# Performance work log

Measured on AMD Instinct MI355X. Metric: run time of the kernel, lower is better.

## Reference

```python
import jax, jax.numpy as jnp
import numpy as np

B, S, E = 8, 4096, 512
QKV, H = 512, 8
D = QKV // H  # head_dim = 64
EPS = 1e-6


def setup_inputs() -> dict:
    key = jax.random.key(0)
    ks = jax.random.split(key, 9)
    sc_in = 1.0 / np.sqrt(E)
    sc_qkv = 1.0 / np.sqrt(QKV)
    # Linear weights stored as [in, out] so y = x @ W + b (equivalent to torch x @ W_t.T + b)
    return {
        "x": jax.random.normal(ks[0], (B, S, E), dtype=jnp.float32),
        "Wq": jax.random.uniform(ks[1], (E, QKV), jnp.float32, -sc_in, sc_in),
        "bq": jax.random.uniform(ks[2], (QKV,), jnp.float32, -sc_in, sc_in),
        "Wk": jax.random.uniform(ks[3], (E, QKV), jnp.float32, -sc_in, sc_in),
        "bk": jax.random.uniform(ks[4], (QKV,), jnp.float32, -sc_in, sc_in),
        "Wv": jax.random.uniform(ks[5], (E, QKV), jnp.float32, -sc_in, sc_in),
        "bv": jax.random.uniform(ks[6], (QKV,), jnp.float32, -sc_in, sc_in),
        "Wo": jax.random.uniform(ks[7], (QKV, E), jnp.float32, -sc_qkv, sc_qkv),
        "bo": jax.random.uniform(ks[8], (E,), jnp.float32, -sc_qkv, sc_qkv),
    }


def feature_map(t):
    # elu(x) + 1 (always positive features)
    return jax.nn.elu(t) + 1.0


def reference(x, Wq, bq, Wk, bk, Wv, bv, Wo, bo):
    bs, seqlen, _ = x.shape
    q = (x @ Wq + bq).reshape(bs, seqlen, H, D)
    k = (x @ Wk + bk).reshape(bs, seqlen, H, D)
    v = (x @ Wv + bv).reshape(bs, seqlen, H, D)
    q = feature_map(q)
    k = feature_map(k)
    # kv: [n, h, m, d] -- per-head outer-product accumulation over sequence
    kv = jnp.einsum('nshd,nshm->nhmd', k, v)
    # normalizer z: [n, l, h]
    z = 1.0 / (jnp.einsum('nlhd,nhd->nlh', q, k.sum(axis=1)) + EPS)
    out = jnp.einsum('nlhd,nhmd,nlh->nlhm', q, kv, z)
    out = out.reshape(bs, seqlen, QKV)
    return out @ Wo + bo
```

## Files before the change

kernel.cpp:

```cpp
#include <hip/hip_runtime.h>
#include <hip/hip_bf16.h>


typedef __bf16 bf16x8 __attribute__((ext_vector_type(8)));
typedef float  f32x4  __attribute__((ext_vector_type(4)));

__device__ __forceinline__ float b2f(unsigned short u) {
    unsigned int x = ((unsigned int)u) << 16;
    return __builtin_bit_cast(float, x);
}
__device__ __forceinline__ unsigned short f2b(float f) {
    unsigned int u = __builtin_bit_cast(unsigned int, f);
    unsigned int r = (u + 0x7FFFu + ((u >> 16) & 1u)) >> 16;
    return (unsigned short)r;
}
__device__ __forceinline__ void load_lds16(const unsigned short* g, unsigned short* l) {
    __builtin_amdgcn_global_load_lds(
        (const __attribute__((address_space(1))) void*)g,
        (__attribute__((address_space(3))) void*)l, 16, 0, 0);
}

__global__ void prep_kernel(const float* __restrict__ x,
                            const float* __restrict__ w0, const float* __restrict__ w1,
                            const float* __restrict__ w2, const float* __restrict__ w3,
                            unsigned short* __restrict__ xb, unsigned short* __restrict__ wt,
                            float* __restrict__ ksg) {
    __shared__ float tile[64][65];
    int t = threadIdx.x;
    if (blockIdx.x >= 256) {
        int i = (blockIdx.x - 256) * 256 + t;
        float4 v = ((const float4*)x)[i];
        ushort4 o;
        o.x = f2b(v.x); o.y = f2b(v.y); o.z = f2b(v.z); o.w = f2b(v.w);
        ((ushort4*)xb)[i] = o;
        return;
    }
    int idx = blockIdx.x;
    if (idx < 16) ksg[idx * 256 + t] = 0.f;
    int bz = idx >> 6, by = (idx >> 3) & 7, bx = idx & 7;
    const float* src = (bz == 0) ? w0 : (bz == 1) ? w1 : (bz == 2) ? w2 : w3;
    unsigned short* dst = wt + (size_t)bz * 512 * 512;
    int rb = by * 64, cb = bx * 64;
    #pragma unroll
    for (int i = 0; i < 16; i++) {
        int c = t + i * 256; int r = c >> 6, cc = c & 63;
        tile[r][cc] = src[(rb + r) * 512 + cb + cc];
    }
    __syncthreads();
    #pragma unroll
    for (int i = 0; i < 16; i++) {
        int c = t + i * 256; int r = c >> 6, cc = c & 63;
        dst[(cb + r) * 512 + rb + cc] = f2b(tile[cc][r]);
    }
}

__global__ __launch_bounds__(256, 4) void gemm_qkv_kernel(
        const unsigned short* __restrict__ xb, const unsigned short* __restrict__ wt,
        const float* __restrict__ bq, const float* __restrict__ bk, const float* __restrict__ bv,
        unsigned short* __restrict__ qb, unsigned short* __restrict__ kT,
        unsigned short* __restrict__ vT, float* __restrict__ ksg) {
    int g = blockIdx.x;
    int xcd = g & 7, slot = g >> 3;
    int mtile = xcd * 32 + slot / 12;
    int tn = slot % 12;
    int tensor = tn >> 2, ntile = tn & 3;
    const unsigned short* Bt = wt + (size_t)tensor * 512 * 512;
    const float* bias = tensor == 0 ? bq : tensor == 1 ? bk : bv;
    bool act = tensor < 2;

    __shared__ __align__(16) unsigned short sA[128 * 64];
    __shared__ __align__(16) unsigned short sB[128 * 64];
    const int tid  = threadIdx.x;
    const int wave = tid >> 6, lane = tid & 63;
    const int wm = wave >> 1, wn = wave & 1;
    const int quad = lane >> 4, l16 = lane & 15;
    const int mbase = mtile * 128, nbase = ntile * 128;
    const int rsub = lane >> 3;
    const int coff = (((lane & 7) ^ rsub) << 3);

    f32x4 acc[4][4];
    #pragma unroll
    for (int i = 0; i < 4; i++)
        #pragma unroll
        for (int j = 0; j < 4; j++) acc[i][j] = (f32x4){0.f, 0.f, 0.f, 0.f};

    for (int kb = 0; kb < 512; kb += 64) {
        #pragma unroll
        for (int t = 0; t < 4; t++) {
            int r0 = t * 32 + wave * 8;
            load_lds16(&xb[(size_t)(mbase + r0 + rsub) * 512 + kb + coff], &sA[r0 * 64]);
            load_lds16(&Bt[(size_t)(nbase + r0 + rsub) * 512 + kb + coff], &sB[r0 * 64]);
        }
        __syncthreads();
        #pragma unroll
        for (int ko = 0; ko < 64; ko += 32) {
            bf16x8 af[4], bfr[4];
            int pg = ((quad + (ko >> 3)) ^ (l16 & 7)) << 3;
            #pragma unroll
            for (int f = 0; f < 4; f++)
                af[f] = *(const bf16x8*)&sA[(wm * 64 + f * 16 + l16) * 64 + pg];
            #pragma unroll
            for (int f = 0; f < 4; f++)
                bfr[f] = *(const bf16x8*)&sB[(wn * 64 + f * 16 + l16) * 64 + pg];
            #pragma unroll
            for (int i = 0; i < 4; i++)
                #pragma unroll
                for (int j = 0; j < 4; j++)
                    acc[i][j] = __builtin_amdgcn_mfma_f32_16x16x32_bf16(af[i], bfr[j], acc[i][j], 0, 0, 0);
        }
        __syncthreads();
    }
    if (tensor == 0) {
        #pragma unroll
        for (int i = 0; i < 4; i++)
            #pragma unroll
            for (int j = 0; j < 4; j++) {
                int gcol = nbase + wn * 64 + j * 16 + l16;
                float bv = bias[gcol];
                #pragma unroll
                for (int r = 0; r < 4; r++) {
                    int grow = mbase + wm * 64 + i * 16 + quad * 4 + r;
                    float v = acc[i][j][r] + bv;
                    v = v > 0.f ? v + 1.f : __expf(v);
                    qb[(size_t)grow * 512 + gcol] = f2b(v);
                }
            }
    } else {
        unsigned short* T = (tensor == 1) ? kT : vT;
        float csum[4] = {0.f, 0.f, 0.f, 0.f};
        #pragma unroll
        for (int i = 0; i < 4; i++)
            #pragma unroll
            for (int j = 0; j < 4; j++) {
                int gcol = nbase + wn * 64 + j * 16 + l16;
                int h = gcol >> 6, d = gcol & 63;
                float bv = bias[gcol];
                int grow0 = mbase + wm * 64 + i * 16 + quad * 4;
                int b = grow0 >> 12, s0 = grow0 & 4095;
                ushort4 o;
                #pragma unroll
                for (int r = 0; r < 4; r++) {
                    float v = acc[i][j][r] + bv;
                    if (act) { v = v > 0.f ? v + 1.f : __expf(v); csum[j] += v; }
                    ((unsigned short*)&o)[r] = f2b(v);
                }
                *(ushort4*)&T[(((size_t)b * 8 + h) * 64 + d) * 4096 + s0] = o;
            }
        if (act) {
            int b = mbase >> 12;
            #pragma unroll
            for (int j = 0; j < 4; j++) {
                float s = csum[j];
                s += __shfl_xor(s, 16, 64);
                s += __shfl_xor(s, 32, 64);
                if (quad == 0) {
                    int gcol = nbase + wn * 64 + j * 16 + l16;
                    atomicAdd(&ksg[b * 512 + gcol], s);
                }
            }
        }
    }
}

__global__ __launch_bounds__(256, 4) void kv_kernel(
        const unsigned short* __restrict__ kT, const unsigned short* __restrict__ vT,
        float* __restrict__ kvp) {
    int bh = blockIdx.x >> 3, sc = blockIdx.x & 7;
    const int tid = threadIdx.x;
    const int wave = tid >> 6, lane = tid & 63;
    const int wm = wave >> 1, wn = wave & 1;
    const int quad = lane >> 4, l16 = lane & 15;
    const int rsub = lane >> 3;
    const int coff = (((lane & 7) ^ rsub) << 3);
    __shared__ __align__(16) unsigned short sV[64 * 64];
    __shared__ __align__(16) unsigned short sK[64 * 64];

    f32x4 acc[2][2];
    #pragma unroll
    for (int i = 0; i < 2; i++)
        #pragma unroll
        for (int j = 0; j < 2; j++) acc[i][j] = (f32x4){0.f, 0.f, 0.f, 0.f};
    size_t base = (size_t)bh * 64 * 4096 + sc * 512;

    for (int kb = 0; kb < 8; kb++) {
        int s0 = kb * 64;
        #pragma unroll
        for (int t = 0; t < 2; t++) {
            int r0 = t * 32 + wave * 8;
            load_lds16(&vT[base + (size_t)(r0 + rsub) * 4096 + s0 + coff], &sV[r0 * 64]);
            load_lds16(&kT[base + (size_t)(r0 + rsub) * 4096 + s0 + coff], &sK[r0 * 64]);
        }
        __syncthreads();
        #pragma unroll
        for (int ko = 0; ko < 64; ko += 32) {
            bf16x8 af[2], bfr[2];
            int pg = ((quad + (ko >> 3)) ^ (l16 & 7)) << 3;
            #pragma unroll
            for (int f = 0; f < 2; f++)
                af[f] = *(const bf16x8*)&sV[(wm * 32 + f * 16 + l16) * 64 + pg];
            #pragma unroll
            for (int f = 0; f < 2; f++)
                bfr[f] = *(const bf16x8*)&sK[(wn * 32 + f * 16 + l16) * 64 + pg];
            #pragma unroll
            for (int i = 0; i < 2; i++)
                #pragma unroll
                for (int j = 0; j < 2; j++)
                    acc[i][j] = __builtin_amdgcn_mfma_f32_16x16x32_bf16(af[i], bfr[j], acc[i][j], 0, 0, 0);
        }
        __syncthreads();
    }
    float* kvout = kvp + ((size_t)sc * 64 + bh) * 4096;
    #pragma unroll
    for (int i = 0; i < 2; i++)
        #pragma unroll
        for (int j = 0; j < 2; j++)
            #pragma unroll
            for (int r = 0; r < 4; r++) {
                int m = wm * 32 + i * 16 + quad * 4 + r;
                int d = wn * 32 + j * 16 + l16;
                kvout[m * 64 + d] = acc[i][j][r];
            }
}

__global__ __launch_bounds__(256) void mid_kernel(
        const float* __restrict__ kvp, unsigned short* __restrict__ kvb) {
    int bh = blockIdx.x >> 2, part = blockIdx.x & 3;
    int tid = threadIdx.x;
    int idx = (part * 256 + tid) * 4;
    float s0 = 0.f, s1 = 0.f, s2 = 0.f, s3 = 0.f;
    #pragma unroll
    for (int sc = 0; sc < 8; sc++) {
        float4 v = *(const float4*)&kvp[((size_t)sc * 64 + bh) * 4096 + idx];
        s0 += v.x; s1 += v.y; s2 += v.z; s3 += v.w;
    }
    ushort4 o; o.x = f2b(s0); o.y = f2b(s1); o.z = f2b(s2); o.w = f2b(s3);
    *(ushort4*)&kvb[(size_t)bh * 4096 + idx] = o;
}

__global__ __launch_bounds__(256, 2) void fused_out_kernel(
        const unsigned short* __restrict__ qb,
        const unsigned short* __restrict__ kvb, const float* __restrict__ ksg,
        const unsigned short* __restrict__ wto, const float* __restrict__ bo,
        float* __restrict__ out) {
    int g = blockIdx.x;
    int xcd = g & 7, slot = g >> 3;
    int mtile = xcd * 32 + (slot >> 1);
    int np = slot & 1;

    __shared__ __align__(16) unsigned short sQ[128 * 64];
    __shared__ __align__(16) unsigned short sWo[2][128 * 64];
    __shared__ __align__(16) unsigned short sKV[64 * 64];
    __shared__ __align__(16) unsigned short sO1[128 * 64];
    __shared__ float sKsum[512];
    __shared__ float sZ[128];
    const int tid  = threadIdx.x;
    const int wave = tid >> 6, lane = tid & 63;
    const int wm = wave >> 1, wn = wave & 1;
    const int quad = lane >> 4, l16 = lane & 15;
    const int mbase = mtile * 128, nbase = np * 256;
    const int b = mtile >> 5;
    const int rsub = lane >> 3;
    const int coff = (((lane & 7) ^ rsub) << 3);

    sKsum[tid]       = ksg[b * 512 + tid];
    sKsum[tid + 256] = ksg[b * 512 + 256 + tid];

    f32x4 accm[2][4][4];
    #pragma unroll
    for (int n = 0; n < 2; n++)
        #pragma unroll
        for (int i = 0; i < 4; i++)
            #pragma unroll
            for (int j = 0; j < 4; j++) accm[n][i][j] = (f32x4){0.f, 0.f, 0.f, 0.f};

    for (int h = 0; h < 8; h++) {
        #pragma unroll
        for (int t = 0; t < 4; t++) {
            int r0 = t * 32 + wave * 8;
            load_lds16(&qb[(size_t)(mbase + r0 + rsub) * 512 + h * 64 + coff], &sQ[r0 * 64]);
            load_lds16(&wto[(size_t)(nbase + r0 + rsub) * 512 + h * 64 + coff], &sWo[0][r0 * 64]);
            load_lds16(&wto[(size_t)(nbase + 128 + r0 + rsub) * 512 + h * 64 + coff], &sWo[1][r0 * 64]);
        }
        #pragma unroll
        for (int t = 0; t < 2; t++) {
            int r0 = t * 32 + wave * 8;
            load_lds16(&kvb[(size_t)(b * 8 + h) * 4096 + (r0 + rsub) * 64 + coff], &sKV[r0 * 64]);
        }
        __syncthreads();
        {
            int row = tid >> 1, half = tid & 1;
            const float* ksh = &sKsum[h * 64];
            float dsum = 0.f;
            #pragma unroll
            for (int g2 = 0; g2 < 4; g2++) {
                int G = half * 4 + g2;
                uint4 w = *(const uint4*)&sQ[row * 64 + ((G ^ (row & 7)) << 3)];
                const unsigned int* qp = (const unsigned int*)&w;
                #pragma unroll
                for (int u = 0; u < 4; u++) {
                    int c = G * 8 + u * 2;
                    dsum += __builtin_bit_cast(float, qp[u] << 16)        * ksh[c];
                    dsum += __builtin_bit_cast(float, qp[u] & 0xFFFF0000u) * ksh[c + 1];
                }
            }
            dsum += __shfl_xor(dsum, 1, 64);
            if (!half) sZ[row] = 1.f / (dsum + 1e-6f);
        }
        __syncthreads();
        f32x4 acco[4][2];
        #pragma unroll
        for (int f = 0; f < 4; f++)
            #pragma unroll
            for (int j = 0; j < 2; j++) acco[f][j] = (f32x4){0.f, 0.f, 0.f, 0.f};
        #pragma unroll
        for (int ko = 0; ko < 64; ko += 32) {
            bf16x8 af[4], bfr[2];
            int pg = ((quad + (ko >> 3)) ^ (l16 & 7)) << 3;
            #pragma unroll
            for (int f = 0; f < 4; f++)
                af[f] = *(const bf16x8*)&sQ[(wm * 64 + f * 16 + l16) * 64 + pg];
            #pragma unroll
            for (int j = 0; j < 2; j++)
                bfr[j] = *(const bf16x8*)&sKV[(wn * 32 + j * 16 + l16) * 64 + pg];
            #pragma unroll
            for (int f = 0; f < 4; f++)
                #pragma unroll
                for (int j = 0; j < 2; j++)
                    acco[f][j] = __builtin_amdgcn_mfma_f32_16x16x32_bf16(af[f], bfr[j], acco[f][j], 0, 0, 0);
        }
        #pragma unroll
        for (int f = 0; f < 4; f++)
            #pragma unroll
            for (int j = 0; j < 2; j++)
                #pragma unroll
                for (int r = 0; r < 4; r++) {
                    int row = wm * 64 + f * 16 + quad * 4 + r;
                    int col = wn * 32 + j * 16 + l16;
                    float v = acco[f][j][r] * sZ[row];
                    int grp = col >> 3;
                    sO1[row * 64 + ((grp ^ (row & 7)) << 3) + (col & 7)] = f2b(v);
                }
        __syncthreads();
        #pragma unroll
        for (int ko = 0; ko < 64; ko += 32) {
            bf16x8 af[4], bfr0[4], bfr1[4];
            int pg = ((quad + (ko >> 3)) ^ (l16 & 7)) << 3;
            #pragma unroll
            for (int f = 0; f < 4; f++)
                af[f] = *(const bf16x8*)&sO1[(wm * 64 + f * 16 + l16) * 64 + pg];
            #pragma unroll
            for (int f = 0; f < 4; f++) {
                bfr0[f] = *(const bf16x8*)&sWo[0][(wn * 64 + f * 16 + l16) * 64 + pg];
                bfr1[f] = *(const bf16x8*)&sWo[1][(wn * 64 + f * 16 + l16) * 64 + pg];
            }
            #pragma unroll
            for (int i = 0; i < 4; i++)
                #pragma unroll
                for (int j = 0; j < 4; j++) {
                    accm[0][i][j] = __builtin_amdgcn_mfma_f32_16x16x32_bf16(af[i], bfr0[j], accm[0][i][j], 0, 0, 0);
                    accm[1][i][j] = __builtin_amdgcn_mfma_f32_16x16x32_bf16(af[i], bfr1[j], accm[1][i][j], 0, 0, 0);
                }
        }
        __syncthreads();
    }
    #pragma unroll
    for (int n = 0; n < 2; n++)
        #pragma unroll
        for (int i = 0; i < 4; i++)
            #pragma unroll
            for (int j = 0; j < 4; j++) {
                int gcol = nbase + n * 128 + wn * 64 + j * 16 + l16;
                float bv = bo[gcol];
                #pragma unroll
                for (int r = 0; r < 4; r++) {
                    int grow = mbase + wm * 64 + i * 16 + quad * 4 + r;
                    out[(size_t)grow * 512 + gcol] = accm[n][i][j][r] + bv;
                }
            }
}

extern "C" void kernel_launch(void* const* d_in, const int* in_sizes, int n_in,
                              void* d_out, int out_size, void* d_ws, size_t ws_size,
                              hipStream_t stream) {
    const float* x  = (const float*)d_in[0];
    const float* Wq = (const float*)d_in[1];
    const float* bq = (const float*)d_in[2];
    const float* Wk = (const float*)d_in[3];
    const float* bk = (const float*)d_in[4];
    const float* Wv = (const float*)d_in[5];
    const float* bv = (const float*)d_in[6];
    const float* Wo = (const float*)d_in[7];
    const float* bo = (const float*)d_in[8];
    float* out = (float*)d_out;

    char* wsb = (char*)d_ws;
    char* ob  = (char*)d_out;
    unsigned short* vT  = (unsigned short*)ob;
    unsigned short* xb  = (unsigned short*)(ob + 33554432ull);
    float*          kvp = (float*)(ob + 33554432ull);
    unsigned short* qb  = (unsigned short*)wsb;
    unsigned short* kT  = (unsigned short*)(wsb + 33554432ull);
    unsigned short* wt  = (unsigned short*)(wsb + 67108864ull);
    unsigned short* kvb = (unsigned short*)(wsb + 69206016ull);
    float*          ksg = (float*)(wsb + 69730304ull);

    prep_kernel<<<16640, 256, 0, stream>>>(x, Wq, Wk, Wv, Wo, xb, wt, ksg);
    gemm_qkv_kernel<<<3072, 256, 0, stream>>>(xb, wt, bq, bk, bv, qb, kT, vT, ksg);
    kv_kernel<<<512, 256, 0, stream>>>(kT, vT, kvp);
    mid_kernel<<<256, 256, 0, stream>>>(kvp, kvb);
    fused_out_kernel<<<512, 256, 0, stream>>>(qb, kvb, ksg,
            wt + 3ull * 512 * 512, bo, out);
}
```

Measured before the change: 242.5 us.

## Atomically reduce KV partials, drop mid kernel, double-buffer kv_kernel loads

The kv_kernel now accumulates its per-chunk partial KV products straight into a zeroed fp32 global buffer with atomicAdd. This removes the separate mid_kernel reduction launch and the intermediate partial buffer. The fused output kernel converts the fp32 KV to bf16 while staging it into LDS. kv_kernel also double-buffers its LDS tiles with explicit waitcnt and barriers so the next chunk's loads overlap compute. The costs are atomic contention (8 chunks per bh), a register-path load instead of a direct LDS load, and non-deterministic summation order.

```diff
diff --git a/kernel.cpp b/kernel.cpp
--- a/kernel.cpp
+++ b/kernel.cpp
@@ -24,7 +24,7 @@
                             const float* __restrict__ w0, const float* __restrict__ w1,
                             const float* __restrict__ w2, const float* __restrict__ w3,
                             unsigned short* __restrict__ xb, unsigned short* __restrict__ wt,
-                            float* __restrict__ ksg) {
+                            float* __restrict__ ksg, float* __restrict__ kvg) {
     __shared__ float tile[64][65];
     int t = threadIdx.x;
     if (blockIdx.x >= 256) {
@@ -37,6 +37,7 @@
     }
     int idx = blockIdx.x;
     if (idx < 16) ksg[idx * 256 + t] = 0.f;
+    ((float4*)kvg)[idx * 256 + t] = (float4){0.f, 0.f, 0.f, 0.f};
     int bz = idx >> 6, by = (idx >> 3) & 7, bx = idx & 7;
     const float* src = (bz == 0) ? w0 : (bz == 1) ? w1 : (bz == 2) ? w2 : w3;
     unsigned short* dst = wt + (size_t)bz * 512 * 512;
@@ -162,9 +163,9 @@
     }
 }
 
-__global__ __launch_bounds__(256, 4) void kv_kernel(
+__global__ __launch_bounds__(256, 2) void kv_kernel(
         const unsigned short* __restrict__ kT, const unsigned short* __restrict__ vT,
-        float* __restrict__ kvp) {
+        float* __restrict__ kvg) {
     int bh = blockIdx.x >> 3, sc = blockIdx.x & 7;
     const int tid = threadIdx.x;
     const int wave = tid >> 6, lane = tid & 63;
@@ -172,8 +173,8 @@
     const int quad = lane >> 4, l16 = lane & 15;
     const int rsub = lane >> 3;
     const int coff = (((lane & 7) ^ rsub) << 3);
-    __shared__ __align__(16) unsigned short sV[64 * 64];
-    __shared__ __align__(16) unsigned short sK[64 * 64];
+    __shared__ __align__(16) unsigned short sV[2][64 * 64];
+    __shared__ __align__(16) unsigned short sK[2][64 * 64];
 
     f32x4 acc[2][2];
     #pragma unroll
@@ -182,34 +183,47 @@
         for (int j = 0; j < 2; j++) acc[i][j] = (f32x4){0.f, 0.f, 0.f, 0.f};
     size_t base = (size_t)bh * 64 * 4096 + sc * 512;
 
-    for (int kb = 0; kb < 8; kb++) {
+    auto stage = [&](int kb, int buf) {
         int s0 = kb * 64;
         #pragma unroll
         for (int t = 0; t < 2; t++) {
             int r0 = t * 32 + wave * 8;
-            load_lds16(&vT[base + (size_t)(r0 + rsub) * 4096 + s0 + coff], &sV[r0 * 64]);
-            load_lds16(&kT[base + (size_t)(r0 + rsub) * 4096 + s0 + coff], &sK[r0 * 64]);
-        }
-        __syncthreads();
+            load_lds16(&vT[base + (size_t)(r0 + rsub) * 4096 + s0 + coff], &sV[buf][r0 * 64]);
+            load_lds16(&kT[base + (size_t)(r0 + rsub) * 4096 + s0 + coff], &sK[buf][r0 * 64]);
+        }
+    };
+
+    stage(0, 0);
+    for (int kb = 0; kb < 8; kb++) {
+        int buf = kb & 1;
+        if (kb < 7) {
+            stage(kb + 1, buf ^ 1);
+            asm volatile("s_waitcnt vmcnt(4)" ::: "memory");
+        } else {
+            asm volatile("s_waitcnt vmcnt(0)" ::: "memory");
+        }
+        __builtin_amdgcn_sched_barrier(0);
+        __builtin_amdgcn_s_barrier();
         #pragma unroll
         for (int ko = 0; ko < 64; ko += 32) {
             bf16x8 af[2], bfr[2];
             int pg = ((quad + (ko >> 3)) ^ (l16 & 7)) << 3;
             #pragma unroll
             for (int f = 0; f < 2; f++)
-                af[f] = *(const bf16x8*)&sV[(wm * 32 + f * 16 + l16) * 64 + pg];
+                af[f] = *(const bf16x8*)&sV[buf][(wm * 32 + f * 16 + l16) * 64 + pg];
             #pragma unroll
             for (int f = 0; f < 2; f++)
-                bfr[f] = *(const bf16x8*)&sK[(wn * 32 + f * 16 + l16) * 64 + pg];
+                bfr[f] = *(const bf16x8*)&sK[buf][(wn * 32 + f * 16 + l16) * 64 + pg];
             #pragma unroll
             for (int i = 0; i < 2; i++)
                 #pragma unroll
                 for (int j = 0; j < 2; j++)
                     acc[i][j] = __builtin_amdgcn_mfma_f32_16x16x32_bf16(af[i], bfr[j], acc[i][j], 0, 0, 0);
         }
-        __syncthreads();
-    }
-    float* kvout = kvp + ((size_t)sc * 64 + bh) * 4096;
+        __builtin_amdgcn_s_barrier();
+        __builtin_amdgcn_sched_barrier(0);
+    }
+    float* out = kvg + (size_t)bh * 4096;
     #pragma unroll
     for (int i = 0; i < 2; i++)
         #pragma unroll
@@ -218,28 +232,13 @@
             for (int r = 0; r < 4; r++) {
                 int m = wm * 32 + i * 16 + quad * 4 + r;
                 int d = wn * 32 + j * 16 + l16;
-                kvout[m * 64 + d] = acc[i][j][r];
-            }
-}
-
-__global__ __launch_bounds__(256) void mid_kernel(
-        const float* __restrict__ kvp, unsigned short* __restrict__ kvb) {
-    int bh = blockIdx.x >> 2, part = blockIdx.x & 3;
-    int tid = threadIdx.x;
-    int idx = (part * 256 + tid) * 4;
-    float s0 = 0.f, s1 = 0.f, s2 = 0.f, s3 = 0.f;
-    #pragma unroll
-    for (int sc = 0; sc < 8; sc++) {
-        float4 v = *(const float4*)&kvp[((size_t)sc * 64 + bh) * 4096 + idx];
-        s0 += v.x; s1 += v.y; s2 += v.z; s3 += v.w;
-    }
-    ushort4 o; o.x = f2b(s0); o.y = f2b(s1); o.z = f2b(s2); o.w = f2b(s3);
-    *(ushort4*)&kvb[(size_t)bh * 4096 + idx] = o;
+                atomicAdd(&out[m * 64 + d], acc[i][j][r]);
+            }
 }
 
 __global__ __launch_bounds__(256, 2) void fused_out_kernel(
         const unsigned short* __restrict__ qb,
-        const unsigned short* __restrict__ kvb, const float* __restrict__ ksg,
+        const float* __restrict__ kvg, const float* __restrict__ ksg,
         const unsigned short* __restrict__ wto, const float* __restrict__ bo,
         float* __restrict__ out) {
     int g = blockIdx.x;
@@ -282,9 +281,16 @@
             load_lds16(&wto[(size_t)(nbase + 128 + r0 + rsub) * 512 + h * 64 + coff], &sWo[1][r0 * 64]);
         }
         #pragma unroll
-        for (int t = 0; t < 2; t++) {
-            int r0 = t * 32 + wave * 8;
-            load_lds16(&kvb[(size_t)(b * 8 + h) * 4096 + (r0 + rsub) * 64 + coff], &sKV[r0 * 64]);
+        for (int oi = 0; oi < 2; oi++) {
+            int idx = tid + oi * 256;
+            int row = idx >> 3, G = idx & 7;
+            const float4* src = (const float4*)&kvg[((size_t)(b * 8 + h)) * 4096 + row * 64 + G * 8];
+            float4 a = src[0], c = src[1];
+            unsigned int p0 = (unsigned int)f2b(a.x) | ((unsigned int)f2b(a.y) << 16);
+            unsigned int p1 = (unsigned int)f2b(a.z) | ((unsigned int)f2b(a.w) << 16);
+            unsigned int p2 = (unsigned int)f2b(c.x) | ((unsigned int)f2b(c.y) << 16);
+            unsigned int p3 = (unsigned int)f2b(c.z) | ((unsigned int)f2b(c.w) << 16);
+            *(uint4*)&sKV[row * 64 + ((G ^ (row & 7)) << 3)] = (uint4){p0, p1, p2, p3};
         }
         __syncthreads();
         {
@@ -397,17 +403,15 @@
     char* ob  = (char*)d_out;
     unsigned short* vT  = (unsigned short*)ob;
     unsigned short* xb  = (unsigned short*)(ob + 33554432ull);
-    float*          kvp = (float*)(ob + 33554432ull);
     unsigned short* qb  = (unsigned short*)wsb;
     unsigned short* kT  = (unsigned short*)(wsb + 33554432ull);
     unsigned short* wt  = (unsigned short*)(wsb + 67108864ull);
-    unsigned short* kvb = (unsigned short*)(wsb + 69206016ull);
-    float*          ksg = (float*)(wsb + 69730304ull);
-
-    prep_kernel<<<16640, 256, 0, stream>>>(x, Wq, Wk, Wv, Wo, xb, wt, ksg);
+    float*          kvg = (float*)(wsb + 69206016ull);
+    float*          ksg = (float*)(wsb + 70254592ull);
+
+    prep_kernel<<<16640, 256, 0, stream>>>(x, Wq, Wk, Wv, Wo, xb, wt, ksg, kvg);
     gemm_qkv_kernel<<<3072, 256, 0, stream>>>(xb, wt, bq, bk, bv, qb, kT, vT, ksg);
-    kv_kernel<<<512, 256, 0, stream>>>(kT, vT, kvp);
-    mid_kernel<<<256, 256, 0, stream>>>(kvp, kvb);
-    fused_out_kernel<<<512, 256, 0, stream>>>(qb, kvb, ksg,
+    kv_kernel<<<512, 256, 0, stream>>>(kT, vT, kvg);
+    fused_out_kernel<<<512, 256, 0, stream>>>(qb, kvg, ksg,
             wt + 3ull * 512 * 512, bo, out);
 }
```

Result: slower. 249.2 us (+2.8%).
